# Kernel optimization log

Hardware: AMD Instinct MI355X
Metric: run time of the kernel (lower is better)

## Reference

```python
import jax, jax.numpy as jnp
import numpy as np

B, L, DIM, NH = 32, 512, 256, 4
HD = DIM // NH  # head_size = 64
SCALE = float(np.sqrt(HD))


def setup_inputs() -> dict:
    key = jax.random.key(0)
    k1, k2, k3, k4 = jax.random.split(key, 4)
    x = jax.random.normal(k1, (B, L, DIM), dtype=jnp.float32)
    adj = jax.random.randint(k2, (B, L, L), 0, 16, dtype=jnp.int32)
    w_qkv = jax.random.normal(k3, (3 * DIM, DIM), dtype=jnp.float32) * 0.02
    w_proj = jax.random.normal(k4, (DIM, DIM), dtype=jnp.float32) * 0.02
    return {"x": x, "adj": adj, "w_qkv": w_qkv, "w_proj": w_proj}


def reference(x, adj, w_qkv, w_proj):
    # qkv projection (torch Linear, no bias: y = x @ W.T)
    qkv = x @ w_qkv.T  # [B, L, 3*DIM]
    q, k, v = jnp.split(qkv, 3, axis=-1)
    q = q.reshape(B, L, NH, HD).transpose(0, 2, 1, 3)  # [B, H, L, HD]
    k = k.reshape(B, L, NH, HD).transpose(0, 2, 1, 3)
    v = v.reshape(B, L, NH, HD).transpose(0, 2, 1, 3)

    score = jnp.einsum('bhqd,bhkd->bhqk', q, k) / SCALE  # [B, H, L, L]

    # rel_pos_bias adjacency mask construction
    a = jnp.where((adj > 1) & (adj < 9), 0, adj)
    a = (a != 0).astype(jnp.float32)               # binarized adjacency [B, L, L]
    aT = jnp.swapaxes(a, -1, -2)
    pe = jnp.stack([a, aT, aT @ a, a @ aT], axis=1)  # [B, 4, L, L]
    pe = pe + jnp.eye(L, dtype=jnp.float32)
    pe = pe.astype(jnp.int32)

    score = jnp.where(pe == 0, -jnp.inf, score)
    attn = jax.nn.softmax(score, axis=-1)
    out = jnp.einsum('bhqk,bhkd->bhqd', attn, v)   # [B, H, L, HD]
    out = out.transpose(0, 2, 1, 3).reshape(B, L, DIM)
    return out @ w_proj.T
```

## Files before the change

### kernel.cpp

```cpp
#include <hip/hip_runtime.h>


typedef unsigned long long u64;
typedef unsigned short u16;
typedef short bf16x8 __attribute__((ext_vector_type(8)));
typedef float f32x4 __attribute__((ext_vector_type(4)));

#define MFMA16(a, b, c) __builtin_amdgcn_mfma_f32_16x16x32_bf16((a), (b), (c), 0, 0, 0)

__device__ __forceinline__ unsigned f2bf(float f) {
  unsigned u = __float_as_uint(f);
  return (u + 0x7FFFu + ((u >> 16) & 1u)) >> 16;
}
__device__ __forceinline__ float bf2f(unsigned b) { return __uint_as_float(b << 16); }

__device__ __forceinline__ unsigned cvtpk(float lo, float hi) {
  unsigned r;
  asm("v_cvt_pk_bf16_f32 %0, %1, %2" : "=v"(r) : "v"(lo), "v"(hi));
  return r;
}

__device__ __forceinline__ void gload16(const u16* src, u16* ldsDst) {
  __builtin_amdgcn_global_load_lds(
      (const __attribute__((address_space(1))) void*)src,
      (__attribute__((address_space(3))) void*)ldsDst, 16, 0, 0);
}

__device__ __forceinline__ int swzE(int row, int e) {
  return row * 64 + (e ^ ((row & 7) << 3));
}
__device__ __forceinline__ int swzV(int row, int c) {
  return row * 512 + (c ^ ((row & 7) << 3));
}

#define OFF_XB    ((size_t)0)
#define OFF_WQKV  ((size_t)8388608)
#define OFF_WPA   ((size_t)8781824)
#define OFF_QB    ((size_t)9175040)
#define OFF_KB    ((size_t)17563648)
#define OFF_VTB   ((size_t)25952256)
#define OFF_CTXA  ((size_t)34340864)
#define OFF_ROWR  ((size_t)51118080)
#define OFF_COLR  ((size_t)52166656)
#define OFF_MASK  ((size_t)53215232)

__global__ __launch_bounds__(512) void prep(const float* __restrict__ x, u16* __restrict__ xb,
                                            const float* __restrict__ wqkv, u16* __restrict__ wqkvb,
                                            const float* __restrict__ wp, u16* __restrict__ wpa,
                                            const int* __restrict__ adj, u64* __restrict__ rowraw,
                                            u64* __restrict__ maskA0) {
  int blk = blockIdx.x;
  if (blk < 1072) {
    const float* src = (blk < 1024) ? x : wqkv;
    u16* dst = (blk < 1024) ? xb : wqkvb;
    int bb = (blk < 1024) ? blk : (blk - 1024);
    size_t i = ((size_t)bb * 512 + threadIdx.x) * 8;
    float4 a = *(const float4*)(src + i);
    float4 c = *(const float4*)(src + i + 4);
    uint4 o;
    o.x = f2bf(a.x) | (f2bf(a.y) << 16);
    o.y = f2bf(a.z) | (f2bf(a.w) << 16);
    o.z = f2bf(c.x) | (f2bf(c.y) << 16);
    o.w = f2bf(c.z) | (f2bf(c.w) << 16);
    *(uint4*)(dst + i) = o;
  } else if (blk < 1200) {
    int idx = (blk - 1072) * 512 + threadIdx.x;
    int n = idx >> 8, k = idx & 255;
    float v = wp[idx];
    unsigned hi = f2bf(v);
    unsigned lo = f2bf(v - bf2f(hi));
    size_t base = (size_t)n * 768;
    wpa[base + k]       = (u16)hi;
    wpa[base + 256 + k] = (u16)hi;
    wpa[base + 512 + k] = (u16)lo;
  } else {
    int blk2 = blk - 1200;
    int b = blk2 >> 6, r0 = (blk2 & 63) * 8;
    int wave = threadIdx.x >> 6, lane = threadIdx.x & 63;
    #pragma unroll
    for (int rr = 0; rr < 8; ++rr) {
      int row = r0 + rr;
      int v = adj[((size_t)b * 512 + row) * 512 + wave * 64 + lane];
      u64 bal = __ballot(v == 1 || v >= 9);
      if (lane == 0) {
        size_t o = ((size_t)b * 512 + row) * 8 + wave;
        rowraw[o] = bal;
        maskA0[o] = bal | (((row >> 6) == wave) ? (1ull << (row & 63)) : 0ull);
      }
    }
  }
}

__global__ __launch_bounds__(512) void transposeW(const u64* __restrict__ rowraw,
                                                  u64* __restrict__ colraw,
                                                  u64* __restrict__ maskA1) {
  const int b = blockIdx.x, wd = blockIdx.y;
  const int tid = threadIdx.x, w = tid >> 6, t = tid & 63;
  u64 rw = rowraw[(size_t)b * 4096 + (size_t)(wd * 64 + t) * 8 + w];
  u64 mine = 0;
  #pragma unroll 1
  for (int cbit = 0; cbit < 64; ++cbit) {
    u64 bal = __ballot((rw >> cbit) & 1ull);
    if (t == cbit) mine = bal;
  }
  int col = w * 64 + t;
  size_t o = (size_t)b * 4096 + (size_t)col * 8 + wd;
  colraw[o] = mine;
  u64 eye = (w == wd) ? (1ull << t) : 0ull;
  maskA1[o] = mine | eye;
}

__global__ __launch_bounds__(512) void maskp(const u64* __restrict__ rowraw,
                                             const u64* __restrict__ colraw,
                                             u64* __restrict__ maskA2,
                                             u64* __restrict__ maskA3) {
  __shared__ u64 rows[512][9];
  const int b = blockIdx.x, w = blockIdx.y, type = blockIdx.z;
  const int tid = threadIdx.x, wavid = tid >> 6, lane = tid & 63;
  const u64* src = type ? rowraw : colraw;
  u64* dst = type ? maskA3 : maskA2;
  {
    const u64* s = src + (size_t)b * 4096 + (size_t)tid * 8;
    #pragma unroll
    for (int k = 0; k < 8; ++k) rows[tid][k] = s[k];
  }
  __syncthreads();
  u64 jr[8];
  #pragma unroll
  for (int k = 0; k < 8; ++k) jr[k] = rows[w * 64 + lane][k];
  #pragma unroll 4
  for (int qq = 0; qq < 64; ++qq) {
    int q = wavid * 64 + qq;
    u64 x = 0;
    #pragma unroll
    for (int k = 0; k < 8; ++k) x |= jr[k] & rows[q][k];
    u64 word = __ballot(x != 0ull);
    if (lane == qq) {
      u64 eye = (wavid == w) ? (1ull << qq) : 0ull;
      dst[(size_t)b * 4096 + (size_t)q * 8 + w] = word | eye;
    }
  }
}

__global__ __launch_bounds__(256) void gemm_qkv(const u16* __restrict__ A,
                                                const u16* __restrict__ Bw,
                                                u16* __restrict__ o_q, u16* __restrict__ o_k,
                                                u16* __restrict__ o_v) {
  __shared__ u16 As[128 * 64];
  __shared__ u16 Bs[128 * 64];
  const int lin = blockIdx.x;
  const int logical = (lin & 7) * 96 + (lin >> 3);
  const int m0 = (logical / 6) * 128, n0 = (logical % 6) * 128;
  const int tid = threadIdx.x;
  const int lane = tid & 63, wid = tid >> 6;
  const int lg = lane >> 4, lc = lane & 15;
  const int wm = wid >> 1, wn = wid & 1;
  f32x4 acc[4][4] = {};

  const int srow = lane >> 3;
  const int schunk = ((lane & 7) ^ srow) * 8;
  #define STAGE_QKV(ks)                                                        \
    {                                                                          \
      int kk0 = (ks) * 64;                                                     \
      _Pragma("unroll")                                                        \
      for (int j = 0; j < 4; ++j) {                                            \
        int slab = wid * 4 + j;                                                \
        int r = slab * 8 + srow;                                               \
        gload16(A + (size_t)(m0 + r) * 256 + kk0 + schunk, &As[slab * 512]);   \
        gload16(Bw + (size_t)(n0 + r) * 256 + kk0 + schunk, &Bs[slab * 512]);  \
      }                                                                        \
    }

  STAGE_QKV(0);
  for (int ks = 0; ks < 4; ++ks) {
    __syncthreads();
    bf16x8 af[2][4], bf[2][4];
    #pragma unroll
    for (int kk = 0; kk < 2; ++kk)
      #pragma unroll
      for (int mi = 0; mi < 4; ++mi) {
        af[kk][mi] = *(const bf16x8*)&As[swzE(wm * 64 + mi * 16 + lc, kk * 32 + lg * 8)];
        bf[kk][mi] = *(const bf16x8*)&Bs[swzE(wn * 64 + mi * 16 + lc, kk * 32 + lg * 8)];
      }
    __syncthreads();
    if (ks < 3) STAGE_QKV(ks + 1);
    #pragma unroll
    for (int kk = 0; kk < 2; ++kk)
      #pragma unroll
      for (int mi = 0; mi < 4; ++mi)
        #pragma unroll
        for (int ni = 0; ni < 4; ++ni)
          acc[mi][ni] = MFMA16(af[kk][mi], bf[kk][ni], acc[mi][ni]);
  }
  #undef STAGE_QKV

  #pragma unroll
  for (int mi = 0; mi < 4; ++mi) {
    int mbase = m0 + wm * 64 + mi * 16 + lg * 4;
    int bb = mbase >> 9, l = mbase & 511;
    #pragma unroll
    for (int ni = 0; ni < 4; ++ni) {
      int n = n0 + wn * 64 + ni * 16 + lc;
      if (n < 512) {
        u16* dst = (n < 256) ? o_q : o_k;
        int c = n & 255, hh = c >> 6, dd = c & 63;
        size_t base = (((size_t)bb * 4 + hh) * 512 + l) * 64 + dd;
        #pragma unroll
        for (int r = 0; r < 4; ++r) dst[base + (size_t)r * 64] = (u16)f2bf(acc[mi][ni][r]);
      } else {
        int c = n - 512, hh = c >> 6, dd = c & 63;
        ushort4 pk;
        pk.x = (u16)f2bf(acc[mi][ni][0]); pk.y = (u16)f2bf(acc[mi][ni][1]);
        pk.z = (u16)f2bf(acc[mi][ni][2]); pk.w = (u16)f2bf(acc[mi][ni][3]);
        *(ushort4*)&o_v[(((size_t)bb * 4 + hh) * 64 + dd) * 512 + l] = pk;
      }
    }
  }
}

__global__ __launch_bounds__(256) void gemm_out(const u16* __restrict__ A,
                                                const u16* __restrict__ Bw,
                                                float* __restrict__ o_f) {
  __shared__ u16 As[64 * 64];
  __shared__ u16 Bs[128 * 64];
  const int lin = blockIdx.x;
  const int logical = (lin & 7) * 64 + (lin >> 3);
  const int m0 = (logical >> 1) * 64, n0 = (logical & 1) * 128;
  const int tid = threadIdx.x;
  const int lane = tid & 63, wid = tid >> 6;
  const int lg = lane >> 4, lc = lane & 15;
  const int wm = wid >> 1, wn = wid & 1;
  f32x4 acc[2][4] = {};

  const int srow = lane >> 3;
  const int schunk = ((lane & 7) ^ srow) * 8;
  #define STAGE_OUT(ks)                                                        \
    {                                                                          \
      int k0 = (ks) * 64;                                                      \
      int ka0 = (k0 >= 512) ? k0 - 512 : k0;                                   \
      _Pragma("unroll")                                                        \
      for (int j = 0; j < 2; ++j) {                                            \
        int slab = wid * 2 + j;                                                \
        int r = slab * 8 + srow;                                               \
        gload16(A + (size_t)(m0 + r) * 512 + ka0 + schunk, &As[slab * 512]);   \
      }                                                                        \
      _Pragma("unroll")                                                        \
      for (int j = 0; j < 4; ++j) {                                            \
        int slab = wid * 4 + j;                                                \
        int r = slab * 8 + srow;                                               \
        gload16(Bw + (size_t)(n0 + r) * 768 + k0 + schunk, &Bs[slab * 512]);   \
      }                                                                        \
    }

  STAGE_OUT(0);
  for (int ks = 0; ks < 12; ++ks) {
    __syncthreads();
    bf16x8 af[2][2], bf[2][4];
    #pragma unroll
    for (int kk = 0; kk < 2; ++kk) {
      #pragma unroll
      for (int mi = 0; mi < 2; ++mi)
        af[kk][mi] = *(const bf16x8*)&As[swzE(wm * 32 + mi * 16 + lc, kk * 32 + lg * 8)];
      #pragma unroll
      for (int ni = 0; ni < 4; ++ni)
        bf[kk][ni] = *(const bf16x8*)&Bs[swzE(wn * 64 + ni * 16 + lc, kk * 32 + lg * 8)];
    }
    __syncthreads();
    if (ks < 11) STAGE_OUT(ks + 1);
    #pragma unroll
    for (int kk = 0; kk < 2; ++kk)
      #pragma unroll
      for (int mi = 0; mi < 2; ++mi)
        #pragma unroll
        for (int ni = 0; ni < 4; ++ni)
          acc[mi][ni] = MFMA16(af[kk][mi], bf[kk][ni], acc[mi][ni]);
  }
  #undef STAGE_OUT

  #pragma unroll
  for (int mi = 0; mi < 2; ++mi) {
    int mbase = m0 + wm * 32 + mi * 16 + lg * 4;
    #pragma unroll
    for (int ni = 0; ni < 4; ++ni) {
      int n = n0 + wn * 64 + ni * 16 + lc;
      #pragma unroll
      for (int r = 0; r < 4; ++r) o_f[(size_t)(mbase + r) * 256 + n] = acc[mi][ni][r];
    }
  }
}

__device__ __forceinline__ void p_step(const f32x4 sT[4], u64 mw, int lane, u16* PsW,
                                       float& lrun, bf16x8& ap0, bf16x8& ap1) {
  const float SC = 0.125f * 1.4426950408889634f;
  const int lg = lane >> 4, lc = lane & 15;
  float p[4][4];
  float ps = 0.f;
  #pragma unroll
  for (int nf = 0; nf < 4; ++nf)
    #pragma unroll
    for (int r = 0; r < 4; ++r) {
      bool ok = (mw >> (nf * 16 + r)) & 1ull;
      float e = __builtin_amdgcn_exp2f(sT[nf][r] * SC);
      e = ok ? e : 0.f;
      p[nf][r] = e;
      ps += e;
    }
  lrun += ps;

  #pragma unroll
  for (int nf = 0; nf < 4; ++nf) {
    uint2 w2;
    w2.x = cvtpk(p[nf][0], p[nf][1]);
    w2.y = cvtpk(p[nf][2], p[nf][3]);
    *(uint2*)&PsW[swzE(lc, nf * 16 + lg * 4)] = w2;
  }
  ap0 = *(const bf16x8*)&PsW[swzE(lc, lg * 8)];
  ap1 = *(const bf16x8*)&PsW[swzE(lc, lg * 8 + 32)];
}

__global__ __launch_bounds__(512, 1) void attn(const u16* __restrict__ qb, const u16* __restrict__ kb,
                                               const u16* __restrict__ vtb, const u64* __restrict__ maskA,
                                               u16* __restrict__ ctxa) {
  __shared__ u16 Ks[512 * 64];
  __shared__ u16 Vs[64 * 512];
  __shared__ u16 Ps[8][16 * 64];
  const int lin = blockIdx.x;
  const int logical = (lin & 7) * 32 + (lin >> 3);
  const int bh = logical >> 1, half = logical & 1;
  const int b = bh >> 2, h = bh & 3;
  const int tid = threadIdx.x, lane = tid & 63, wid = tid >> 6;
  const int lg = lane >> 4, lc = lane & 15;

  {
    const u16* kgs = kb + (size_t)bh * 512 * 64;
    const u16* vgs = vtb + (size_t)bh * 64 * 512;
    const int srow = lane >> 3;
    const int schunk = ((lane & 7) ^ srow) * 8;
    #pragma unroll
    for (int j = 0; j < 8; ++j) {
      int slab = wid * 8 + j;
      gload16(kgs + (size_t)(slab * 8 + srow) * 64 + schunk, &Ks[slab * 512]);
    }
    #pragma unroll
    for (int j = 0; j < 8; ++j) {
      int vr = wid * 8 + j;
      gload16(vgs + (size_t)vr * 512 + ((lane ^ (vr & 7)) * 8), &Vs[vr * 512]);
    }
  }

  const int qrow0 = half * 256 + wid * 32;
  const u16* qgA = qb + ((size_t)bh * 512 + qrow0 + lc) * 64;
  const u16* qgB = qgA + 16 * 64;
  bf16x8 qA0 = *(const bf16x8*)(qgA + lg * 8);
  bf16x8 qA1 = *(const bf16x8*)(qgA + 32 + lg * 8);
  bf16x8 qB0 = *(const bf16x8*)(qgB + lg * 8);
  bf16x8 qB1 = *(const bf16x8*)(qgB + 32 + lg * 8);

  float lrunA = 0.f, lrunB = 0.f;
  f32x4 accoA[4] = {}, accoB[4] = {};
  const u64* mrowA = maskA + ((size_t)(h * 32 + b) * 512 + qrow0 + lc) * 8;
  const u64* mrowB = mrowA + 16 * 8;
  u16* PsW = Ps[wid];

  u64 mwA = mrowA[0], mwB = mrowB[0];

  __syncthreads();

  for (int kt = 0; kt < 8; ++kt) {
    u64 nmwA = (kt < 7) ? mrowA[kt + 1] : 0ull;
    u64 nmwB = (kt < 7) ? mrowB[kt + 1] : 0ull;

    f32x4 sA[4], sB[4];
    __builtin_amdgcn_s_setprio(1);
    #pragma unroll
    for (int nf = 0; nf < 4; ++nf) {
      bf16x8 ak0 = *(const bf16x8*)&Ks[swzE(kt * 64 + nf * 16 + lc, lg * 8)];
      bf16x8 ak1 = *(const bf16x8*)&Ks[swzE(kt * 64 + nf * 16 + lc, lg * 8 + 32)];
      f32x4 zA = {0.f, 0.f, 0.f, 0.f};
      zA = MFMA16(ak0, qA0, zA);
      zA = MFMA16(ak1, qA1, zA);
      sA[nf] = zA;
      f32x4 zB = {0.f, 0.f, 0.f, 0.f};
      zB = MFMA16(ak0, qB0, zB);
      zB = MFMA16(ak1, qB1, zB);
      sB[nf] = zB;
    }
    __builtin_amdgcn_s_setprio(0);

    bf16x8 apA0, apA1, apB0, apB1;
    p_step(sA, mwA >> (lg * 4), lane, PsW, lrunA, apA0, apA1);
    p_step(sB, mwB >> (lg * 4), lane, PsW, lrunB, apB0, apB1);

    __builtin_amdgcn_s_setprio(1);
    #pragma unroll
    for (int df = 0; df < 4; ++df) {
      bf16x8 bv0 = *(const bf16x8*)&Vs[swzV(df * 16 + lc, kt * 64 + lg * 8)];
      bf16x8 bv1 = *(const bf16x8*)&Vs[swzV(df * 16 + lc, kt * 64 + 32 + lg * 8)];
      accoA[df] = MFMA16(apA0, bv0, accoA[df]);
      accoA[df] = MFMA16(apA1, bv1, accoA[df]);
      accoB[df] = MFMA16(apB0, bv0, accoB[df]);
      accoB[df] = MFMA16(apB1, bv1, accoB[df]);
    }
    __builtin_amdgcn_s_setprio(0);

    mwA = nmwA;
    mwB = nmwB;
  }

  lrunA += __shfl_xor(lrunA, 16);
  lrunA += __shfl_xor(lrunA, 32);
  lrunB += __shfl_xor(lrunB, 16);
  lrunB += __shfl_xor(lrunB, 32);
  float lrA[4], lrB[4];
  #pragma unroll
  for (int r = 0; r < 4; ++r) {
    lrA[r] = 1.0f / __shfl(lrunA, (lane & 48) | (lg * 4 + r));
    lrB[r] = 1.0f / __shfl(lrunB, (lane & 48) | (lg * 4 + r));
  }
  #pragma unroll
  for (int r = 0; r < 4; ++r) {
    int rowq = qrow0 + lg * 4 + r;
    size_t baseA = ((size_t)b * 512 + rowq) * 512;
    size_t baseB = ((size_t)b * 512 + rowq + 16) * 512;
    #pragma unroll
    for (int df = 0; df < 4; ++df) {
      int c = h * 64 + df * 16 + lc;
      float vA = accoA[df][r] * lrA[r];
      unsigned hiA = f2bf(vA);
      ctxa[baseA + c]       = (u16)hiA;
      ctxa[baseA + 256 + c] = (u16)f2bf(vA - bf2f(hiA));
      float vB = accoB[df][r] * lrB[r];
      unsigned hiB = f2bf(vB);
      ctxa[baseB + c]       = (u16)hiB;
      ctxa[baseB + 256 + c] = (u16)f2bf(vB - bf2f(hiB));
    }
  }
}

extern "C" void kernel_launch(void* const* d_in, const int* in_sizes, int n_in,
                              void* d_out, int out_size, void* d_ws, size_t ws_size,
                              hipStream_t stream) {
  const float* x     = (const float*)d_in[0];
  const int*   adj   = (const int*)d_in[1];
  const float* wqkv  = (const float*)d_in[2];
  const float* wproj = (const float*)d_in[3];
  char* ws = (char*)d_ws;
  u16* xb     = (u16*)(ws + OFF_XB);
  u16* wqkvb  = (u16*)(ws + OFF_WQKV);
  u16* wpa    = (u16*)(ws + OFF_WPA);
  u16* qb     = (u16*)(ws + OFF_QB);
  u16* kb     = (u16*)(ws + OFF_KB);
  u16* vtb    = (u16*)(ws + OFF_VTB);
  u16* ctxa   = (u16*)(ws + OFF_CTXA);
  u64* rowraw = (u64*)(ws + OFF_ROWR);
  u64* colraw = (u64*)(ws + OFF_COLR);
  u64* maskA  = (u64*)(ws + OFF_MASK);
  const size_t MSTRIDE = (size_t)32 * 512 * 8;

  prep<<<dim3(3248), 512, 0, stream>>>(x, xb, wqkv, wqkvb, wproj, wpa, adj, rowraw, maskA);
  transposeW<<<dim3(32, 8), 512, 0, stream>>>(rowraw, colraw, maskA + MSTRIDE);
  maskp<<<dim3(32, 8, 2), 512, 0, stream>>>(rowraw, colraw, maskA + 2 * MSTRIDE, maskA + 3 * MSTRIDE);
  gemm_qkv<<<dim3(768), 256, 0, stream>>>(xb, wqkvb, qb, kb, vtb);
  attn<<<dim3(256), 512, 0, stream>>>(qb, kb, vtb, maskA, ctxa);
  gemm_out<<<dim3(512), 256, 0, stream>>>(ctxa, wpa, (float*)d_out);
}
```

Before: 85.99 us.

## Fuse adjacency transpose into mask kernel and split K staging in attention

Merges the separate transposeW kernel into the mask-product kernel: blocks of type 0 rebuild the bit-transposed adjacency in shared memory themselves rather than reading a colraw buffer from global memory, and block w==0 writes maskA1. This removes one launch and a global round trip, at the cost of every type-0 block redoing the full 512x512 bit transpose (redundant work ×8). Separately, the attention kernel now loads V and only the first half of K before the main loop, issues the second-half K loads afterwards, and places a barrier between the two halves of the key loop so those loads can overlap the first-half compute.

```diff
diff --git a/kernel.cpp b/kernel.cpp
--- a/kernel.cpp
+++ b/kernel.cpp
@@ -91,40 +91,55 @@
   }
 }
 
-__global__ __launch_bounds__(512) void transposeW(const u64* __restrict__ rowraw,
-                                                  u64* __restrict__ colraw,
-                                                  u64* __restrict__ maskA1) {
-  const int b = blockIdx.x, wd = blockIdx.y;
-  const int tid = threadIdx.x, w = tid >> 6, t = tid & 63;
-  u64 rw = rowraw[(size_t)b * 4096 + (size_t)(wd * 64 + t) * 8 + w];
-  u64 mine = 0;
-  #pragma unroll 1
-  for (int cbit = 0; cbit < 64; ++cbit) {
-    u64 bal = __ballot((rw >> cbit) & 1ull);
-    if (t == cbit) mine = bal;
-  }
-  int col = w * 64 + t;
-  size_t o = (size_t)b * 4096 + (size_t)col * 8 + wd;
-  colraw[o] = mine;
-  u64 eye = (w == wd) ? (1ull << t) : 0ull;
-  maskA1[o] = mine | eye;
-}
-
-__global__ __launch_bounds__(512) void maskp(const u64* __restrict__ rowraw,
-                                             const u64* __restrict__ colraw,
+__global__ __launch_bounds__(512) void maskc(const u64* __restrict__ rowraw,
+                                             u64* __restrict__ maskA1,
                                              u64* __restrict__ maskA2,
                                              u64* __restrict__ maskA3) {
+  __shared__ u64 btr[8 * 512];
   __shared__ u64 rows[512][9];
   const int b = blockIdx.x, w = blockIdx.y, type = blockIdx.z;
   const int tid = threadIdx.x, wavid = tid >> 6, lane = tid & 63;
-  const u64* src = type ? rowraw : colraw;
   u64* dst = type ? maskA3 : maskA2;
-  {
-    const u64* s = src + (size_t)b * 4096 + (size_t)tid * 8;
+
+  if (type) {
+    const u64* s = rowraw + (size_t)b * 4096 + (size_t)tid * 8;
     #pragma unroll
     for (int k = 0; k < 8; ++k) rows[tid][k] = s[k];
-  }
-  __syncthreads();
+    __syncthreads();
+  } else {
+    {
+      const u64* s = rowraw + (size_t)b * 4096 + (size_t)tid * 8;
+      u64 r[8];
+      #pragma unroll
+      for (int k = 0; k < 8; ++k) r[k] = s[k];
+      #pragma unroll
+      for (int k = 0; k < 8; ++k) btr[k * 512 + tid] = r[k];
+    }
+    __syncthreads();
+    u64 words[8];
+    #pragma unroll
+    for (int wd = 0; wd < 8; ++wd) {
+      u64 word = btr[wavid * 512 + wd * 64 + lane];
+      u64 mine = 0;
+      #pragma unroll 1
+      for (int c = 0; c < 64; ++c) {
+        u64 bal = __ballot((word >> c) & 1ull);
+        if (lane == c) mine = bal;
+      }
+      words[wd] = mine;
+    }
+    int col = wavid * 64 + lane;
+    #pragma unroll
+    for (int wd = 0; wd < 8; ++wd) rows[col][wd] = words[wd];
+    if (w == 0) {
+      words[wavid] |= (1ull << lane);
+      u64* m1 = maskA1 + (size_t)b * 4096 + (size_t)col * 8;
+      #pragma unroll
+      for (int wd = 0; wd < 8; ++wd) m1[wd] = words[wd];
+    }
+    __syncthreads();
+  }
+
   u64 jr[8];
   #pragma unroll
   for (int k = 0; k < 8; ++k) jr[k] = rows[w * 64 + lane][k];
@@ -331,20 +346,21 @@
   const int tid = threadIdx.x, lane = tid & 63, wid = tid >> 6;
   const int lg = lane >> 4, lc = lane & 15;
 
+  const u16* kgs = kb + (size_t)bh * 512 * 64;
+  const int srow = lane >> 3;
+  const int schunk = ((lane & 7) ^ srow) * 8;
+
   {
-    const u16* kgs = kb + (size_t)bh * 512 * 64;
     const u16* vgs = vtb + (size_t)bh * 64 * 512;
-    const int srow = lane >> 3;
-    const int schunk = ((lane & 7) ^ srow) * 8;
-    #pragma unroll
-    for (int j = 0; j < 8; ++j) {
-      int slab = wid * 8 + j;
-      gload16(kgs + (size_t)(slab * 8 + srow) * 64 + schunk, &Ks[slab * 512]);
-    }
     #pragma unroll
     for (int j = 0; j < 8; ++j) {
       int vr = wid * 8 + j;
       gload16(vgs + (size_t)vr * 512 + ((lane ^ (vr & 7)) * 8), &Vs[vr * 512]);
+    }
+    #pragma unroll
+    for (int j = 0; j < 4; ++j) {
+      int slab = wid * 4 + j;
+      gload16(kgs + (size_t)(slab * 8 + srow) * 64 + schunk, &Ks[slab * 512]);
     }
   }
 
@@ -366,45 +382,54 @@
 
   __syncthreads();
 
-  for (int kt = 0; kt < 8; ++kt) {
-    u64 nmwA = (kt < 7) ? mrowA[kt + 1] : 0ull;
-    u64 nmwB = (kt < 7) ? mrowB[kt + 1] : 0ull;
-
-    f32x4 sA[4], sB[4];
-    __builtin_amdgcn_s_setprio(1);
-    #pragma unroll
-    for (int nf = 0; nf < 4; ++nf) {
-      bf16x8 ak0 = *(const bf16x8*)&Ks[swzE(kt * 64 + nf * 16 + lc, lg * 8)];
-      bf16x8 ak1 = *(const bf16x8*)&Ks[swzE(kt * 64 + nf * 16 + lc, lg * 8 + 32)];
-      f32x4 zA = {0.f, 0.f, 0.f, 0.f};
-      zA = MFMA16(ak0, qA0, zA);
-      zA = MFMA16(ak1, qA1, zA);
-      sA[nf] = zA;
-      f32x4 zB = {0.f, 0.f, 0.f, 0.f};
-      zB = MFMA16(ak0, qB0, zB);
-      zB = MFMA16(ak1, qB1, zB);
-      sB[nf] = zB;
-    }
-    __builtin_amdgcn_s_setprio(0);
-
-    bf16x8 apA0, apA1, apB0, apB1;
-    p_step(sA, mwA >> (lg * 4), lane, PsW, lrunA, apA0, apA1);
-    p_step(sB, mwB >> (lg * 4), lane, PsW, lrunB, apB0, apB1);
-
-    __builtin_amdgcn_s_setprio(1);
-    #pragma unroll
-    for (int df = 0; df < 4; ++df) {
-      bf16x8 bv0 = *(const bf16x8*)&Vs[swzV(df * 16 + lc, kt * 64 + lg * 8)];
-      bf16x8 bv1 = *(const bf16x8*)&Vs[swzV(df * 16 + lc, kt * 64 + 32 + lg * 8)];
-      accoA[df] = MFMA16(apA0, bv0, accoA[df]);
-      accoA[df] = MFMA16(apA1, bv1, accoA[df]);
-      accoB[df] = MFMA16(apB0, bv0, accoB[df]);
-      accoB[df] = MFMA16(apB1, bv1, accoB[df]);
-    }
-    __builtin_amdgcn_s_setprio(0);
-
-    mwA = nmwA;
-    mwB = nmwB;
+  #pragma unroll
+  for (int j = 0; j < 4; ++j) {
+    int slab = 32 + wid * 4 + j;
+    gload16(kgs + (size_t)(slab * 8 + srow) * 64 + schunk, &Ks[slab * 512]);
+  }
+
+  for (int hkt = 0; hkt < 2; ++hkt) {
+    for (int kt = hkt * 4; kt < hkt * 4 + 4; ++kt) {
+      u64 nmwA = (kt < 7) ? mrowA[kt + 1] : 0ull;
+      u64 nmwB = (kt < 7) ? mrowB[kt + 1] : 0ull;
+
+      f32x4 sA[4], sB[4];
+      __builtin_amdgcn_s_setprio(1);
+      #pragma unroll
+      for (int nf = 0; nf < 4; ++nf) {
+        bf16x8 ak0 = *(const bf16x8*)&Ks[swzE(kt * 64 + nf * 16 + lc, lg * 8)];
+        bf16x8 ak1 = *(const bf16x8*)&Ks[swzE(kt * 64 + nf * 16 + lc, lg * 8 + 32)];
+        f32x4 zA = {0.f, 0.f, 0.f, 0.f};
+        zA = MFMA16(ak0, qA0, zA);
+        zA = MFMA16(ak1, qA1, zA);
+        sA[nf] = zA;
+        f32x4 zB = {0.f, 0.f, 0.f, 0.f};
+        zB = MFMA16(ak0, qB0, zB);
+        zB = MFMA16(ak1, qB1, zB);
+        sB[nf] = zB;
+      }
+      __builtin_amdgcn_s_setprio(0);
+
+      bf16x8 apA0, apA1, apB0, apB1;
+      p_step(sA, mwA >> (lg * 4), lane, PsW, lrunA, apA0, apA1);
+      p_step(sB, mwB >> (lg * 4), lane, PsW, lrunB, apB0, apB1);
+
+      __builtin_amdgcn_s_setprio(1);
+      #pragma unroll
+      for (int df = 0; df < 4; ++df) {
+        bf16x8 bv0 = *(const bf16x8*)&Vs[swzV(df * 16 + lc, kt * 64 + lg * 8)];
+        bf16x8 bv1 = *(const bf16x8*)&Vs[swzV(df * 16 + lc, kt * 64 + 32 + lg * 8)];
+        accoA[df] = MFMA16(apA0, bv0, accoA[df]);
+        accoA[df] = MFMA16(apA1, bv1, accoA[df]);
+        accoB[df] = MFMA16(apB0, bv0, accoB[df]);
+        accoB[df] = MFMA16(apB1, bv1, accoB[df]);
+      }
+      __builtin_amdgcn_s_setprio(0);
+
+      mwA = nmwA;
+      mwB = nmwB;
+    }
+    if (hkt == 0) __syncthreads();
   }
 
   lrunA += __shfl_xor(lrunA, 16);
@@ -453,13 +478,11 @@
   u16* vtb    = (u16*)(ws + OFF_VTB);
   u16* ctxa   = (u16*)(ws + OFF_CTXA);
   u64* rowraw = (u64*)(ws + OFF_ROWR);
-  u64* colraw = (u64*)(ws + OFF_COLR);
   u64* maskA  = (u64*)(ws + OFF_MASK);
   const size_t MSTRIDE = (size_t)32 * 512 * 8;
 
   prep<<<dim3(3248), 512, 0, stream>>>(x, xb, wqkv, wqkvb, wproj, wpa, adj, rowraw, maskA);
-  transposeW<<<dim3(32, 8), 512, 0, stream>>>(rowraw, colraw, maskA + MSTRIDE);
-  maskp<<<dim3(32, 8, 2), 512, 0, stream>>>(rowraw, colraw, maskA + 2 * MSTRIDE, maskA + 3 * MSTRIDE);
+  maskc<<<dim3(32, 8, 2), 512, 0, stream>>>(rowraw, maskA + MSTRIDE, maskA + 2 * MSTRIDE, maskA + 3 * MSTRIDE);
   gemm_qkv<<<dim3(768), 256, 0, stream>>>(xb, wqkvb, qb, kb, vtb);
   attn<<<dim3(256), 512, 0, stream>>>(qb, kb, vtb, maskA, ctxa);
   gemm_out<<<dim3(512), 256, 0, stream>>>(ctxa, wpa, (float*)d_out);
```

New measurement: 95.86 us. 11.5% more time.
